# Optimization experiments

Hardware: AMD Instinct MI355X
Metric: run time of the kernel (lower is better)

The kernel has to match this reference:

```python
import jax, jax.numpy as jnp
import numpy as np

BN_EPS = 1e-5
D_SLICE = 3  # forward slices last (neighbor) dim to :3 (d=3 in original code)


def _conv_bn_relu(x, W, b, gamma, beta):
    # x: (B, Cin, N, K) ; W: (Cout, Cin) ; 1x1 Conv2d + eval-mode BatchNorm(mean=0, var=1) + ReLU
    y = jnp.einsum('oi,bink->bonk', W, x) + b[:, None, None]
    y = gamma[:, None, None] * (y / jnp.sqrt(1.0 + BN_EPS)) + beta[:, None, None]
    return jax.nn.relu(y)


def setup_inputs() -> dict:
    key = jax.random.key(0)
    ks = jax.random.split(key, 16)
    B, N, K, C = 4, 32768, 16, 64
    mlp = [128, 64, 64]
    cin = C + 4  # feature + relation (diff_xyz 3 + distance 1)
    inp = {
        'src_xyz': jax.random.normal(ks[0], (B, 3, N, K), dtype=jnp.float32),
        'tgt_xyz': jax.random.normal(ks[1], (B, 3, N), dtype=jnp.float32),
        'feature': jax.random.normal(ks[2], (B, C, N, K), dtype=jnp.float32),
    }
    c_prev = cin
    for i, c_out in enumerate(mlp):
        scale = 1.0 / np.sqrt(c_prev)
        inp[f'W{i+1}'] = jax.random.uniform(ks[3 + 4 * i], (c_out, c_prev), minval=-scale, maxval=scale, dtype=jnp.float32)
        inp[f'b{i+1}'] = jax.random.uniform(ks[4 + 4 * i], (c_out,), minval=-scale, maxval=scale, dtype=jnp.float32)
        inp[f'g{i+1}'] = jnp.ones((c_out,), dtype=jnp.float32)
        inp[f'be{i+1}'] = jnp.zeros((c_out,), dtype=jnp.float32)
        c_prev = c_out
    return inp


def reference(src_xyz, tgt_xyz, feature, W1, b1, g1, be1, W2, b2, g2, be2, W3, b3, g3, be3):
    # relation feature on first D_SLICE neighbors (faithful to feature[:,:,:,:d], d=3)
    diff_xyz = src_xyz[:, :, :, :D_SLICE] - tgt_xyz[:, :, :, None]        # (B,3,N,3)
    distance = jnp.sum(diff_xyz ** 2, axis=1, keepdims=True)             # (B,1,N,3)
    x = jnp.concatenate([feature[:, :, :, :D_SLICE], diff_xyz, distance], axis=1)  # (B,C+4,N,3)
    x = _conv_bn_relu(x, W1, b1, g1, be1)
    x = _conv_bn_relu(x, W2, b2, g2, be2)
    x = _conv_bn_relu(x, W3, b3, g3, be3)
    return jnp.sum(x, axis=3)  # reduction='sum' over neighbor dim -> (B,64,N)
```

## Files before the change

### kernel.cpp

```cpp
#include <hip/hip_runtime.h>
#include <math.h>

typedef __attribute__((ext_vector_type(8))) short short8;
typedef __attribute__((ext_vector_type(4))) short short4v;
typedef __attribute__((ext_vector_type(4))) float f32x4;
typedef __attribute__((ext_vector_type(16))) float f32x16;
typedef _Float16 half8 __attribute__((ext_vector_type(8)));

constexpr int BLOCK = 512;
constexpr int B_ = 4, C_ = 64, N_ = 32768, K_ = 16;
constexpr int P_ = 32;
constexpr int NFRAG = 44;
constexpr int BIAS_OFF = NFRAG * 512;

constexpr int ZOFF = 9 * 768;
constexpr int XSZ  = 6920;
constexpr int H2STR = 776;

__device__ __forceinline__ short f16bits(float v) {
    return (short)__builtin_bit_cast(unsigned short, (_Float16)v);
}

__device__ __forceinline__ f32x16 mm32h(half8 a, half8 b, f32x16 c) {
    return __builtin_amdgcn_mfma_f32_32x32x16_f16(a, b, c, 0, 0, 0);
}
__device__ __forceinline__ f32x4 mm16h(half8 a, half8 b, f32x4 c) {
    return __builtin_amdgcn_mfma_f32_16x16x32_f16(a, b, c, 0, 0, 0);
}

__global__ void prep_wfrags(const float* __restrict__ W1, const float* __restrict__ g1,
                            const float* __restrict__ b1, const float* __restrict__ be1,
                            const float* __restrict__ W2, const float* __restrict__ g2,
                            const float* __restrict__ b2, const float* __restrict__ be2,
                            const float* __restrict__ W3, const float* __restrict__ g3,
                            const float* __restrict__ b3, const float* __restrict__ be3,
                            unsigned short* __restrict__ wf)
{
    const int gid = blockIdx.x * 256 + threadIdx.x;
    const float RS = 1.0f / sqrtf(1.0f + 1e-5f);
    const int NT = NFRAG * 64;
    if (gid < NT) {
        const int f = gid >> 6, l = gid & 63;
        const float *W, *g; int CI, co, kb;
        if (f < 20)      { W = W1; g = g1; CI = 68;
                           co = (f / 5) * 32 + (l & 31);        kb = (f % 5) * 16 + (l >> 5) * 8; }
        else if (f < 36) { W = W2; g = g2; CI = 128;
                           co = ((f - 20) / 8) * 32 + (l & 31); kb = ((f - 20) % 8) * 16 + (l >> 5) * 8; }
        else             { W = W3; g = g3; CI = 64;
                           co = ((f - 36) / 2) * 16 + (l & 15); kb = ((f - 36) % 2) * 32 + (l >> 4) * 8; }
        const float gs = g[co] * RS;
        short8 h8;
#pragma unroll
        for (int j = 0; j < 8; ++j) {
            const int k = kb + j;
            const float w = (k < CI) ? W[(size_t)co * CI + k] * gs : 0.0f;
            h8[j] = f16bits(w);
        }
        *reinterpret_cast<short8*>(wf + (size_t)f * 512 + l * 8) = h8;
    } else if (gid < NT + 256) {
        const int c = gid - NT;
        float* fb = reinterpret_cast<float*>(wf + BIAS_OFF);
        if (c < 128)      fb[c] = b1[c] * (g1[c] * RS) + be1[c];
        else if (c < 192) { const int q = c - 128; fb[c] = b2[q] * (g2[q] * RS) + be2[q]; }
        else              { const int q = c - 192; fb[c] = b3[q] * (g3[q] * RS) + be3[q]; }
    }
}

__device__ __forceinline__ half8 ldfrag(const unsigned short* __restrict__ wf,
                                        int f, int l) {
    return __builtin_bit_cast(half8,
        *reinterpret_cast<const short8*>(wf + (size_t)f * 512 + l * 8));
}

__global__ __launch_bounds__(BLOCK, 8)
void mvp_mfma(const float* __restrict__ src, const float* __restrict__ tgt,
              const float* __restrict__ feat,
              const unsigned short* __restrict__ wf,
              float* __restrict__ out)
{
    __shared__ __align__(16) unsigned short xa[XSZ];
    __shared__ __align__(16) unsigned short h1f[16*768];

    const int tid = threadIdx.x;
    const int w   = tid >> 6;
    const int l   = tid & 63;
    const int b   = blockIdx.x >> 10;
    const int n0  = (blockIdx.x & 1023) << 5;

    unsigned short* h2f = xa;

    float4 pf[4];
#pragma unroll
    for (int it = 0; it < 4; ++it) {
        const int idx = tid + it * BLOCK;
        const int c = idx >> 5, p = idx & 31;
        pf[it] = *reinterpret_cast<const float4*>(
            feat + ((size_t)(b*C_ + c) * N_ + (n0 + p)) * K_);
    }
    float rl[6];
    if (tid < 96) {
        const int p = tid & 31, k = tid >> 5, n = n0 + p;
        rl[0] = src[((size_t)(b*3+0)*N_ + n)*K_ + k];
        rl[1] = src[((size_t)(b*3+1)*N_ + n)*K_ + k];
        rl[2] = src[((size_t)(b*3+2)*N_ + n)*K_ + k];
        rl[3] = tgt[(size_t)(b*3+0)*N_ + n];
        rl[4] = tgt[(size_t)(b*3+1)*N_ + n];
        rl[5] = tgt[(size_t)(b*3+2)*N_ + n];
    }

    if (tid < 96) {
        const int o = (8*96 + tid) * 8 + 4;
        *reinterpret_cast<short4v*>(&xa[o]) = short4v{0,0,0,0};
    } else if (tid == 96) {
        *reinterpret_cast<short8*>(xa + ZOFF) = short8{0,0,0,0,0,0,0,0};
    }

#pragma unroll
    for (int it = 0; it < 4; ++it) {
        const int idx = tid + it * BLOCK;
        const int c = idx >> 5, p = idx & 31;
        const float v[3] = {pf[it].x, pf[it].y, pf[it].z};
#pragma unroll
        for (int k = 0; k < 3; ++k)
            xa[((c >> 3)*96 + k*32 + p)*8 + (c & 7)] = (unsigned short)f16bits(v[k]);
    }
    if (tid < 96) {
        const int p = tid & 31, k = tid >> 5;
        const float d0 = rl[0]-rl[3], d1 = rl[1]-rl[4], d2 = rl[2]-rl[5];
        const float d[4] = {d0, d1, d2, d0*d0 + d1*d1 + d2*d2};
        const int base = (8*96 + k*32 + p)*8;
#pragma unroll
        for (int j = 0; j < 4; ++j)
            xa[base + j] = (unsigned short)f16bits(d[j]);
    }
    __syncthreads();

    const int hi32 = l >> 5, c32 = l & 31;
    const int lq = l >> 4, lr = l & 15, rq = lq << 2;
    const float* fb = reinterpret_cast<const float*>(wf + BIAS_OFF);

    {
        const int npass = (w < 4) ? 2 : 1;
        for (int pass = 0; pass < npass; ++pass) {
            const int t = pass ? (8 + w) : w;
            const int m = t / 3, n = t % 3;
            const int col = n*32 + c32;
            half8 ah[5];
#pragma unroll
            for (int ks = 0; ks < 5; ++ks) ah[ks] = ldfrag(wf, m*5 + ks, l);
            f32x16 acc;
#pragma unroll
            for (int j = 0; j < 16; ++j) acc[j] = 0.0f;
#pragma unroll
            for (int ks = 0; ks < 4; ++ks) {
                const int so = ((ks*2 + hi32)*96 + col)*8;
                const half8 bh = __builtin_bit_cast(half8,
                    *reinterpret_cast<const short8*>(&xa[so]));
                acc = mm32h(ah[ks], bh, acc);
            }
            {
                const int so = hi32 ? ZOFF : (8*96 + col)*8;
                const half8 bh = __builtin_bit_cast(half8,
                    *reinterpret_cast<const short8*>(&xa[so]));
                acc = mm32h(ah[4], bh, acc);
            }
#pragma unroll
            for (int g = 0; g < 4; ++g) {
                const int co0 = m*32 + 8*g + 4*hi32;
                const float4 bb = *reinterpret_cast<const float4*>(fb + co0);
                const float bbv[4] = {bb.x, bb.y, bb.z, bb.w};
                short4v h4;
#pragma unroll
                for (int r = 0; r < 4; ++r)
                    h4[r] = f16bits(fmaxf(acc[g*4 + r] + bbv[r], 0.0f));
                const int so = ((m*4 + g)*96 + col)*8 + 4*hi32;
                *reinterpret_cast<short4v*>(&h1f[so]) = h4;
            }
        }
    }
    __syncthreads();

    if (w < 6) {
        const int m = w / 3, n = w % 3;
        const int col = n*32 + c32;
        f32x16 acc;
#pragma unroll
        for (int j = 0; j < 16; ++j) acc[j] = 0.0f;
#pragma unroll
        for (int ks = 0; ks < 8; ++ks) {
            const half8 ah = ldfrag(wf, 20 + m*8 + ks, l);
            const int so = ((ks*2 + hi32)*96 + col)*8;
            const half8 bh = __builtin_bit_cast(half8,
                *reinterpret_cast<const short8*>(&h1f[so]));
            acc = mm32h(ah, bh, acc);
        }
#pragma unroll
        for (int g = 0; g < 4; ++g) {
            const int co0 = m*32 + 8*g + 4*hi32;
            const float4 bb = *reinterpret_cast<const float4*>(fb + 128 + co0);
            const float bbv[4] = {bb.x, bb.y, bb.z, bb.w};
            short4v h4;
#pragma unroll
            for (int r = 0; r < 4; ++r)
                h4[r] = f16bits(fmaxf(acc[g*4 + r] + bbv[r], 0.0f));
            const int so = (m*4 + g)*H2STR + col*8 + 4*hi32;
            *reinterpret_cast<short4v*>(&h2f[so]) = h4;
        }
    }
    __syncthreads();

    {
        const int m = w >> 1, hh = w & 1;
        half8 ah[2];
#pragma unroll
        for (int ks = 0; ks < 2; ++ks) ah[ks] = ldfrag(wf, 36 + m*2 + ks, l);
        f32x4 acc3[3] = {f32x4{0,0,0,0}, f32x4{0,0,0,0}, f32x4{0,0,0,0}};
#pragma unroll
        for (int ks = 0; ks < 2; ++ks) {
#pragma unroll
            for (int t = 0; t < 3; ++t) {
                const int so = (ks*4 + lq)*H2STR + (t*32 + hh*16 + lr)*8;
                const half8 bh = __builtin_bit_cast(half8,
                    *reinterpret_cast<const short8*>(&h2f[so]));
                acc3[t] = mm16h(ah[ks], bh, acc3[t]);
            }
        }
        const int co0 = m*16 + rq;
        const float4 bb = *reinterpret_cast<const float4*>(fb + 192 + co0);
        const float bbv[4] = {bb.x, bb.y, bb.z, bb.w};
#pragma unroll
        for (int r = 0; r < 4; ++r) {
            float s = 0.0f;
#pragma unroll
            for (int t = 0; t < 3; ++t) s += fmaxf(acc3[t][r] + bbv[r], 0.0f);
            out[(size_t)(b*64 + co0 + r) * N_ + n0 + hh*16 + lr] = s;
        }
    }
}

extern "C" void kernel_launch(void* const* d_in, const int* in_sizes, int n_in,
                              void* d_out, int out_size, void* d_ws, size_t ws_size,
                              hipStream_t stream) {
    const float* src  = (const float*)d_in[0];
    const float* tgt  = (const float*)d_in[1];
    const float* feat = (const float*)d_in[2];
    const float* W1 = (const float*)d_in[3];
    const float* b1 = (const float*)d_in[4];
    const float* g1 = (const float*)d_in[5];
    const float* be1= (const float*)d_in[6];
    const float* W2 = (const float*)d_in[7];
    const float* b2 = (const float*)d_in[8];
    const float* g2 = (const float*)d_in[9];
    const float* be2= (const float*)d_in[10];
    const float* W3 = (const float*)d_in[11];
    const float* b3 = (const float*)d_in[12];
    const float* g3 = (const float*)d_in[13];
    const float* be3= (const float*)d_in[14];
    float* out = (float*)d_out;
    unsigned short* wfrag = (unsigned short*)d_ws;

    prep_wfrags<<<12, 256, 0, stream>>>(W1, g1, b1, be1, W2, g2, b2, be2,
                                        W3, g3, b3, be3, wfrag);

    const int grid = B_ * (N_ / P_);
    mvp_mfma<<<grid, BLOCK, 0, stream>>>(src, tgt, feat, wfrag, out);
}
```

Baseline: 137.6 us.

## Process two 32-point tiles per block with all feature loads issued up front

Each block now handles 64 points as two 32-point tiles, and the grid is halved. The global feature, src and tgt loads for both tiles are issued together at kernel start into a double-buffered LDS input area. The three MLP layers then run on each tile in turn. This raises memory-level parallelism per block and spreads the per-block setup over more work, at the cost of more LDS and registers per block and a lower occupancy target in launch bounds (8 to 6).

```diff
diff --git a/kernel.cpp b/kernel.cpp
--- a/kernel.cpp
+++ b/kernel.cpp
@@ -72,34 +72,36 @@
         *reinterpret_cast<const short8*>(wf + (size_t)f * 512 + l * 8));
 }
 
-__global__ __launch_bounds__(BLOCK, 8)
+__global__ __launch_bounds__(BLOCK, 6)
 void mvp_mfma(const float* __restrict__ src, const float* __restrict__ tgt,
               const float* __restrict__ feat,
               const unsigned short* __restrict__ wf,
               float* __restrict__ out)
 {
-    __shared__ __align__(16) unsigned short xa[XSZ];
+    __shared__ __align__(16) unsigned short xa[2][XSZ];
     __shared__ __align__(16) unsigned short h1f[16*768];
 
     const int tid = threadIdx.x;
     const int w   = tid >> 6;
     const int l   = tid & 63;
-    const int b   = blockIdx.x >> 10;
-    const int n0  = (blockIdx.x & 1023) << 5;
-
-    unsigned short* h2f = xa;
-
-    float4 pf[4];
-#pragma unroll
-    for (int it = 0; it < 4; ++it) {
-        const int idx = tid + it * BLOCK;
-        const int c = idx >> 5, p = idx & 31;
-        pf[it] = *reinterpret_cast<const float4*>(
-            feat + ((size_t)(b*C_ + c) * N_ + (n0 + p)) * K_);
-    }
+    const int b   = blockIdx.x >> 9;
+    const int n0  = (blockIdx.x & 511) << 6;
+
+    float4 pf[8];
+#pragma unroll
+    for (int t = 0; t < 2; ++t)
+#pragma unroll
+        for (int it = 0; it < 4; ++it) {
+            const int idx = tid + it * BLOCK;
+            const int c = idx >> 5, p = idx & 31;
+            pf[t*4 + it] = *reinterpret_cast<const float4*>(
+                feat + ((size_t)(b*C_ + c) * N_ + (n0 + t*32 + p)) * K_);
+        }
     float rl[6];
-    if (tid < 96) {
-        const int p = tid & 31, k = tid >> 5, n = n0 + p;
+    int tt = 0, cc = 0;
+    if (tid < 192) {
+        tt = tid / 96; cc = tid % 96;
+        const int p = cc & 31, k = cc >> 5, n = n0 + tt*32 + p;
         rl[0] = src[((size_t)(b*3+0)*N_ + n)*K_ + k];
         rl[1] = src[((size_t)(b*3+1)*N_ + n)*K_ + k];
         rl[2] = src[((size_t)(b*3+2)*N_ + n)*K_ + k];
@@ -110,28 +112,33 @@
 
     if (tid < 96) {
         const int o = (8*96 + tid) * 8 + 4;
-        *reinterpret_cast<short4v*>(&xa[o]) = short4v{0,0,0,0};
+        *reinterpret_cast<short4v*>(&xa[0][o]) = short4v{0,0,0,0};
+        *reinterpret_cast<short4v*>(&xa[1][o]) = short4v{0,0,0,0};
     } else if (tid == 96) {
-        *reinterpret_cast<short8*>(xa + ZOFF) = short8{0,0,0,0,0,0,0,0};
-    }
-
-#pragma unroll
-    for (int it = 0; it < 4; ++it) {
-        const int idx = tid + it * BLOCK;
-        const int c = idx >> 5, p = idx & 31;
-        const float v[3] = {pf[it].x, pf[it].y, pf[it].z};
-#pragma unroll
-        for (int k = 0; k < 3; ++k)
-            xa[((c >> 3)*96 + k*32 + p)*8 + (c & 7)] = (unsigned short)f16bits(v[k]);
-    }
-    if (tid < 96) {
-        const int p = tid & 31, k = tid >> 5;
+        *reinterpret_cast<short8*>(&xa[0][ZOFF]) = short8{0,0,0,0,0,0,0,0};
+        *reinterpret_cast<short8*>(&xa[1][ZOFF]) = short8{0,0,0,0,0,0,0,0};
+    }
+
+#pragma unroll
+    for (int t = 0; t < 2; ++t)
+#pragma unroll
+        for (int it = 0; it < 4; ++it) {
+            const int idx = tid + it * BLOCK;
+            const int c = idx >> 5, p = idx & 31;
+            const float4 f = pf[t*4 + it];
+            const float v[3] = {f.x, f.y, f.z};
+#pragma unroll
+            for (int k = 0; k < 3; ++k)
+                xa[t][((c >> 3)*96 + k*32 + p)*8 + (c & 7)] = (unsigned short)f16bits(v[k]);
+        }
+    if (tid < 192) {
+        const int p = cc & 31, k = cc >> 5;
         const float d0 = rl[0]-rl[3], d1 = rl[1]-rl[4], d2 = rl[2]-rl[5];
         const float d[4] = {d0, d1, d2, d0*d0 + d1*d1 + d2*d2};
         const int base = (8*96 + k*32 + p)*8;
 #pragma unroll
         for (int j = 0; j < 4; ++j)
-            xa[base + j] = (unsigned short)f16bits(d[j]);
+            xa[tt][base + j] = (unsigned short)f16bits(d[j]);
     }
     __syncthreads();
 
@@ -139,101 +146,107 @@
     const int lq = l >> 4, lr = l & 15, rq = lq << 2;
     const float* fb = reinterpret_cast<const float*>(wf + BIAS_OFF);
 
-    {
-        const int npass = (w < 4) ? 2 : 1;
-        for (int pass = 0; pass < npass; ++pass) {
-            const int t = pass ? (8 + w) : w;
-            const int m = t / 3, n = t % 3;
+#pragma unroll 1
+    for (int t = 0; t < 2; ++t) {
+        const unsigned short* xat = &xa[t][0];
+        unsigned short* h2f = &xa[t][0];
+
+        {
+            const int npass = (w < 4) ? 2 : 1;
+            for (int pass = 0; pass < npass; ++pass) {
+                const int tt1 = pass ? (8 + w) : w;
+                const int m = tt1 / 3, n = tt1 % 3;
+                const int col = n*32 + c32;
+                half8 ah[5];
+#pragma unroll
+                for (int ks = 0; ks < 5; ++ks) ah[ks] = ldfrag(wf, m*5 + ks, l);
+                f32x16 acc;
+#pragma unroll
+                for (int j = 0; j < 16; ++j) acc[j] = 0.0f;
+#pragma unroll
+                for (int ks = 0; ks < 4; ++ks) {
+                    const int so = ((ks*2 + hi32)*96 + col)*8;
+                    const half8 bh = __builtin_bit_cast(half8,
+                        *reinterpret_cast<const short8*>(&xat[so]));
+                    acc = mm32h(ah[ks], bh, acc);
+                }
+                {
+                    const int so = hi32 ? ZOFF : (8*96 + col)*8;
+                    const half8 bh = __builtin_bit_cast(half8,
+                        *reinterpret_cast<const short8*>(&xat[so]));
+                    acc = mm32h(ah[4], bh, acc);
+                }
+#pragma unroll
+                for (int g = 0; g < 4; ++g) {
+                    const int co0 = m*32 + 8*g + 4*hi32;
+                    const float4 bb = *reinterpret_cast<const float4*>(fb + co0);
+                    const float bbv[4] = {bb.x, bb.y, bb.z, bb.w};
+                    short4v h4;
+#pragma unroll
+                    for (int r = 0; r < 4; ++r)
+                        h4[r] = f16bits(fmaxf(acc[g*4 + r] + bbv[r], 0.0f));
+                    const int so = ((m*4 + g)*96 + col)*8 + 4*hi32;
+                    *reinterpret_cast<short4v*>(&h1f[so]) = h4;
+                }
+            }
+        }
+        __syncthreads();
+
+        if (w < 6) {
+            const int m = w / 3, n = w % 3;
             const int col = n*32 + c32;
-            half8 ah[5];
-#pragma unroll
-            for (int ks = 0; ks < 5; ++ks) ah[ks] = ldfrag(wf, m*5 + ks, l);
             f32x16 acc;
 #pragma unroll
             for (int j = 0; j < 16; ++j) acc[j] = 0.0f;
 #pragma unroll
-            for (int ks = 0; ks < 4; ++ks) {
+            for (int ks = 0; ks < 8; ++ks) {
+                const half8 ah = ldfrag(wf, 20 + m*8 + ks, l);
                 const int so = ((ks*2 + hi32)*96 + col)*8;
                 const half8 bh = __builtin_bit_cast(half8,
-                    *reinterpret_cast<const short8*>(&xa[so]));
-                acc = mm32h(ah[ks], bh, acc);
-            }
-            {
-                const int so = hi32 ? ZOFF : (8*96 + col)*8;
-                const half8 bh = __builtin_bit_cast(half8,
-                    *reinterpret_cast<const short8*>(&xa[so]));
-                acc = mm32h(ah[4], bh, acc);
+                    *reinterpret_cast<const short8*>(&h1f[so]));
+                acc = mm32h(ah, bh, acc);
             }
 #pragma unroll
             for (int g = 0; g < 4; ++g) {
                 const int co0 = m*32 + 8*g + 4*hi32;
-                const float4 bb = *reinterpret_cast<const float4*>(fb + co0);
+                const float4 bb = *reinterpret_cast<const float4*>(fb + 128 + co0);
                 const float bbv[4] = {bb.x, bb.y, bb.z, bb.w};
                 short4v h4;
 #pragma unroll
                 for (int r = 0; r < 4; ++r)
                     h4[r] = f16bits(fmaxf(acc[g*4 + r] + bbv[r], 0.0f));
-                const int so = ((m*4 + g)*96 + col)*8 + 4*hi32;
-                *reinterpret_cast<short4v*>(&h1f[so]) = h4;
-            }
-        }
-    }
-    __syncthreads();
-
-    if (w < 6) {
-        const int m = w / 3, n = w % 3;
-        const int col = n*32 + c32;
-        f32x16 acc;
-#pragma unroll
-        for (int j = 0; j < 16; ++j) acc[j] = 0.0f;
-#pragma unroll
-        for (int ks = 0; ks < 8; ++ks) {
-            const half8 ah = ldfrag(wf, 20 + m*8 + ks, l);
-            const int so = ((ks*2 + hi32)*96 + col)*8;
-            const half8 bh = __builtin_bit_cast(half8,
-                *reinterpret_cast<const short8*>(&h1f[so]));
-            acc = mm32h(ah, bh, acc);
-        }
-#pragma unroll
-        for (int g = 0; g < 4; ++g) {
-            const int co0 = m*32 + 8*g + 4*hi32;
-            const float4 bb = *reinterpret_cast<const float4*>(fb + 128 + co0);
+                const int so = (m*4 + g)*H2STR + col*8 + 4*hi32;
+                *reinterpret_cast<short4v*>(&h2f[so]) = h4;
+            }
+        }
+        __syncthreads();
+
+        {
+            const int m = w >> 1, hh = w & 1;
+            half8 ah[2];
+#pragma unroll
+            for (int ks = 0; ks < 2; ++ks) ah[ks] = ldfrag(wf, 36 + m*2 + ks, l);
+            f32x4 acc3[3] = {f32x4{0,0,0,0}, f32x4{0,0,0,0}, f32x4{0,0,0,0}};
+#pragma unroll
+            for (int ks = 0; ks < 2; ++ks) {
+#pragma unroll
+                for (int tk = 0; tk < 3; ++tk) {
+                    const int so = (ks*4 + lq)*H2STR + (tk*32 + hh*16 + lr)*8;
+                    const half8 bh = __builtin_bit_cast(half8,
+                        *reinterpret_cast<const short8*>(&h2f[so]));
+                    acc3[tk] = mm16h(ah[ks], bh, acc3[tk]);
+                }
+            }
+            const int co0 = m*16 + rq;
+            const float4 bb = *reinterpret_cast<const float4*>(fb + 192 + co0);
             const float bbv[4] = {bb.x, bb.y, bb.z, bb.w};
-            short4v h4;
-#pragma unroll
-            for (int r = 0; r < 4; ++r)
-                h4[r] = f16bits(fmaxf(acc[g*4 + r] + bbv[r], 0.0f));
-            const int so = (m*4 + g)*H2STR + col*8 + 4*hi32;
-            *reinterpret_cast<short4v*>(&h2f[so]) = h4;
-        }
-    }
-    __syncthreads();
-
-    {
-        const int m = w >> 1, hh = w & 1;
-        half8 ah[2];
-#pragma unroll
-        for (int ks = 0; ks < 2; ++ks) ah[ks] = ldfrag(wf, 36 + m*2 + ks, l);
-        f32x4 acc3[3] = {f32x4{0,0,0,0}, f32x4{0,0,0,0}, f32x4{0,0,0,0}};
-#pragma unroll
-        for (int ks = 0; ks < 2; ++ks) {
-#pragma unroll
-            for (int t = 0; t < 3; ++t) {
-                const int so = (ks*4 + lq)*H2STR + (t*32 + hh*16 + lr)*8;
-                const half8 bh = __builtin_bit_cast(half8,
-                    *reinterpret_cast<const short8*>(&h2f[so]));
-                acc3[t] = mm16h(ah[ks], bh, acc3[t]);
-            }
-        }
-        const int co0 = m*16 + rq;
-        const float4 bb = *reinterpret_cast<const float4*>(fb + 192 + co0);
-        const float bbv[4] = {bb.x, bb.y, bb.z, bb.w};
-#pragma unroll
-        for (int r = 0; r < 4; ++r) {
-            float s = 0.0f;
-#pragma unroll
-            for (int t = 0; t < 3; ++t) s += fmaxf(acc3[t][r] + bbv[r], 0.0f);
-            out[(size_t)(b*64 + co0 + r) * N_ + n0 + hh*16 + lr] = s;
+#pragma unroll
+            for (int r = 0; r < 4; ++r) {
+                float s = 0.0f;
+#pragma unroll
+                for (int tk = 0; tk < 3; ++tk) s += fmaxf(acc3[tk][r] + bbv[r], 0.0f);
+                out[(size_t)(b*64 + co0 + r) * N_ + n0 + t*32 + hh*16 + lr] = s;
+            }
         }
     }
 }
@@ -262,6 +275,6 @@
     prep_wfrags<<<12, 256, 0, stream>>>(W1, g1, b1, be1, W2, g2, b2, be2,
                                         W3, g3, b3, be3, wfrag);
 
-    const int grid = B_ * (N_ / P_);
+    const int grid = B_ * (N_ / 64);
     mvp_mfma<<<grid, BLOCK, 0, stream>>>(src, tgt, feat, wfrag, out);
 }
```

Result: slower. 242.2 us (+76.0%).

## Split fused kernel into input-packing kernel and MLP kernel via workspace

Applied to the files above, without the earlier changes.

Splits the single fused kernel into two. The first gathers features and relation terms, converts them to fp16 and writes them to global workspace already in the MFMA fragment layout. The second reads that packed layout straight from global memory as the B operand of the first layer and runs the three MFMA layers. The aim is to separate the latency-bound gather from the compute, at the cost of an extra global round-trip of about 15 KB per block plus a second launch. The fused path is kept as a fallback when the workspace is too small.

```diff
diff --git a/kernel.cpp b/kernel.cpp
--- a/kernel.cpp
+++ b/kernel.cpp
@@ -17,10 +17,13 @@
 constexpr int XSZ  = 6920;
 constexpr int H2STR = 776;
 
+constexpr int XG_SHORTS = 10 * 96 * 8;
+constexpr size_t XG_OFF = 65536;
+constexpr int NBLK = B_ * (N_ / P_);
+
 __device__ __forceinline__ short f16bits(float v) {
     return (short)__builtin_bit_cast(unsigned short, (_Float16)v);
 }
-
 __device__ __forceinline__ f32x16 mm32h(half8 a, half8 b, f32x16 c) {
     return __builtin_amdgcn_mfma_f32_32x32x16_f16(a, b, c, 0, 0, 0);
 }
@@ -73,6 +76,176 @@
 }
 
 __global__ __launch_bounds__(BLOCK, 8)
+void prep_x(const float* __restrict__ src, const float* __restrict__ tgt,
+            const float* __restrict__ feat, unsigned short* __restrict__ xg)
+{
+    __shared__ __align__(16) unsigned short xa[XG_SHORTS];
+
+    const int tid = threadIdx.x;
+    const int b   = blockIdx.x >> 10;
+    const int n0  = (blockIdx.x & 1023) << 5;
+
+    float4 pf[4];
+#pragma unroll
+    for (int it = 0; it < 4; ++it) {
+        const int idx = tid + it * BLOCK;
+        const int c = idx >> 5, p = idx & 31;
+        pf[it] = *reinterpret_cast<const float4*>(
+            feat + ((size_t)(b*C_ + c) * N_ + (n0 + p)) * K_);
+    }
+    float rl[6];
+    if (tid < 96) {
+        const int p = tid & 31, k = tid >> 5, n = n0 + p;
+        rl[0] = src[((size_t)(b*3+0)*N_ + n)*K_ + k];
+        rl[1] = src[((size_t)(b*3+1)*N_ + n)*K_ + k];
+        rl[2] = src[((size_t)(b*3+2)*N_ + n)*K_ + k];
+        rl[3] = tgt[(size_t)(b*3+0)*N_ + n];
+        rl[4] = tgt[(size_t)(b*3+1)*N_ + n];
+        rl[5] = tgt[(size_t)(b*3+2)*N_ + n];
+    }
+    if (tid < 96) {
+        *reinterpret_cast<short4v*>(&xa[(8*96 + tid)*8 + 4]) = short4v{0,0,0,0};
+        *reinterpret_cast<short8*>(&xa[(9*96 + tid)*8])      = short8{0,0,0,0,0,0,0,0};
+    }
+#pragma unroll
+    for (int it = 0; it < 4; ++it) {
+        const int idx = tid + it * BLOCK;
+        const int c = idx >> 5, p = idx & 31;
+        const float v[3] = {pf[it].x, pf[it].y, pf[it].z};
+#pragma unroll
+        for (int k = 0; k < 3; ++k)
+            xa[((c >> 3)*96 + k*32 + p)*8 + (c & 7)] = (unsigned short)f16bits(v[k]);
+    }
+    if (tid < 96) {
+        const int p = tid & 31, k = tid >> 5;
+        const float d0 = rl[0]-rl[3], d1 = rl[1]-rl[4], d2 = rl[2]-rl[5];
+        const float d[4] = {d0, d1, d2, d0*d0 + d1*d1 + d2*d2};
+        const int base = (8*96 + k*32 + p)*8;
+#pragma unroll
+        for (int j = 0; j < 4; ++j)
+            xa[base + j] = (unsigned short)f16bits(d[j]);
+    }
+    __syncthreads();
+
+    short8* dst = reinterpret_cast<short8*>(xg + (size_t)blockIdx.x * XG_SHORTS);
+    const short8* srcv = reinterpret_cast<const short8*>(xa);
+    for (int i = tid; i < XG_SHORTS/8; i += BLOCK) dst[i] = srcv[i];
+}
+
+__global__ __launch_bounds__(BLOCK, 8)
+void mvp_mlp(const unsigned short* __restrict__ xg,
+             const unsigned short* __restrict__ wf,
+             float* __restrict__ out)
+{
+    __shared__ __align__(16) unsigned short h1f[16*768];
+    __shared__ __align__(16) unsigned short h2f[6208];
+
+    const int tid = threadIdx.x;
+    const int w   = tid >> 6;
+    const int l   = tid & 63;
+    const int b   = blockIdx.x >> 10;
+    const int n0  = (blockIdx.x & 1023) << 5;
+
+    const unsigned short* xb = xg + (size_t)blockIdx.x * XG_SHORTS;
+
+    const int hi32 = l >> 5, c32 = l & 31;
+    const int lq = l >> 4, lr = l & 15, rq = lq << 2;
+    const float* fb = reinterpret_cast<const float*>(wf + BIAS_OFF);
+
+    {
+        const int npass = (w < 4) ? 2 : 1;
+        for (int pass = 0; pass < npass; ++pass) {
+            const int t = pass ? (8 + w) : w;
+            const int m = t / 3, n = t % 3;
+            const int col = n*32 + c32;
+            half8 ah[5];
+#pragma unroll
+            for (int ks = 0; ks < 5; ++ks) ah[ks] = ldfrag(wf, m*5 + ks, l);
+            f32x16 acc;
+#pragma unroll
+            for (int j = 0; j < 16; ++j) acc[j] = 0.0f;
+#pragma unroll
+            for (int ks = 0; ks < 5; ++ks) {
+                const int so = ((ks*2 + hi32)*96 + col)*8;
+                const half8 bh = __builtin_bit_cast(half8,
+                    *reinterpret_cast<const short8*>(&xb[so]));
+                acc = mm32h(ah[ks], bh, acc);
+            }
+#pragma unroll
+            for (int g = 0; g < 4; ++g) {
+                const int co0 = m*32 + 8*g + 4*hi32;
+                const float4 bb = *reinterpret_cast<const float4*>(fb + co0);
+                const float bbv[4] = {bb.x, bb.y, bb.z, bb.w};
+                short4v h4;
+#pragma unroll
+                for (int r = 0; r < 4; ++r)
+                    h4[r] = f16bits(fmaxf(acc[g*4 + r] + bbv[r], 0.0f));
+                const int so = ((m*4 + g)*96 + col)*8 + 4*hi32;
+                *reinterpret_cast<short4v*>(&h1f[so]) = h4;
+            }
+        }
+    }
+    __syncthreads();
+
+    if (w < 6) {
+        const int m = w / 3, n = w % 3;
+        const int col = n*32 + c32;
+        f32x16 acc;
+#pragma unroll
+        for (int j = 0; j < 16; ++j) acc[j] = 0.0f;
+#pragma unroll
+        for (int ks = 0; ks < 8; ++ks) {
+            const half8 ah = ldfrag(wf, 20 + m*8 + ks, l);
+            const int so = ((ks*2 + hi32)*96 + col)*8;
+            const half8 bh = __builtin_bit_cast(half8,
+                *reinterpret_cast<const short8*>(&h1f[so]));
+            acc = mm32h(ah, bh, acc);
+        }
+#pragma unroll
+        for (int g = 0; g < 4; ++g) {
+            const int co0 = m*32 + 8*g + 4*hi32;
+            const float4 bb = *reinterpret_cast<const float4*>(fb + 128 + co0);
+            const float bbv[4] = {bb.x, bb.y, bb.z, bb.w};
+            short4v h4;
+#pragma unroll
+            for (int r = 0; r < 4; ++r)
+                h4[r] = f16bits(fmaxf(acc[g*4 + r] + bbv[r], 0.0f));
+            const int so = (m*4 + g)*H2STR + col*8 + 4*hi32;
+            *reinterpret_cast<short4v*>(&h2f[so]) = h4;
+        }
+    }
+    __syncthreads();
+
+    {
+        const int m = w >> 1, hh = w & 1;
+        half8 ah[2];
+#pragma unroll
+        for (int ks = 0; ks < 2; ++ks) ah[ks] = ldfrag(wf, 36 + m*2 + ks, l);
+        f32x4 acc3[3] = {f32x4{0,0,0,0}, f32x4{0,0,0,0}, f32x4{0,0,0,0}};
+#pragma unroll
+        for (int ks = 0; ks < 2; ++ks) {
+#pragma unroll
+            for (int t = 0; t < 3; ++t) {
+                const int so = (ks*4 + lq)*H2STR + (t*32 + hh*16 + lr)*8;
+                const half8 bh = __builtin_bit_cast(half8,
+                    *reinterpret_cast<const short8*>(&h2f[so]));
+                acc3[t] = mm16h(ah[ks], bh, acc3[t]);
+            }
+        }
+        const int co0 = m*16 + rq;
+        const float4 bb = *reinterpret_cast<const float4*>(fb + 192 + co0);
+        const float bbv[4] = {bb.x, bb.y, bb.z, bb.w};
+#pragma unroll
+        for (int r = 0; r < 4; ++r) {
+            float s = 0.0f;
+#pragma unroll
+            for (int t = 0; t < 3; ++t) s += fmaxf(acc3[t][r] + bbv[r], 0.0f);
+            out[(size_t)(b*64 + co0 + r) * N_ + n0 + hh*16 + lr] = s;
+        }
+    }
+}
+
+__global__ __launch_bounds__(BLOCK, 8)
 void mvp_mfma(const float* __restrict__ src, const float* __restrict__ tgt,
               const float* __restrict__ feat,
               const unsigned short* __restrict__ wf,
@@ -107,14 +280,12 @@
         rl[4] = tgt[(size_t)(b*3+1)*N_ + n];
         rl[5] = tgt[(size_t)(b*3+2)*N_ + n];
     }
-
     if (tid < 96) {
         const int o = (8*96 + tid) * 8 + 4;
         *reinterpret_cast<short4v*>(&xa[o]) = short4v{0,0,0,0};
     } else if (tid == 96) {
         *reinterpret_cast<short8*>(xa + ZOFF) = short8{0,0,0,0,0,0,0,0};
     }
-
 #pragma unroll
     for (int it = 0; it < 4; ++it) {
         const int idx = tid + it * BLOCK;
@@ -262,6 +433,12 @@
     prep_wfrags<<<12, 256, 0, stream>>>(W1, g1, b1, be1, W2, g2, b2, be2,
                                         W3, g3, b3, be3, wfrag);
 
-    const int grid = B_ * (N_ / P_);
-    mvp_mfma<<<grid, BLOCK, 0, stream>>>(src, tgt, feat, wfrag, out);
-}
+    const size_t need = XG_OFF + (size_t)NBLK * XG_SHORTS * 2;
+    if (ws_size >= need) {
+        unsigned short* xg = (unsigned short*)((char*)d_ws + XG_OFF);
+        prep_x<<<NBLK, BLOCK, 0, stream>>>(src, tgt, feat, xg);
+        mvp_mlp<<<NBLK, BLOCK, 0, stream>>>(xg, wfrag, out);
+    } else {
+        mvp_mfma<<<NBLK, BLOCK, 0, stream>>>(src, tgt, feat, wfrag, out);
+    }
+}
```

Result: slower. 170.6 us (+24.0%).

## Chain MLP layers in registers via lane shuffles, drop intermediate LDS stages

Applied to the files above, without the earlier changes.

Each block now handles 64 points, and each wave owns 32 columns (8 points × 4 padded neighbor slots) for all three layers. Layer outputs are repacked from MFMA accumulator layout into B-operand layout with cross-half-wave shuffles, so the h1/h2 shared-memory buffers and two barriers go away. Layer 3 switches to 32x32 MFMA, and the neighbor sum is done with lane shuffles. This trades some wasted compute on a padded fourth neighbor slot, plus more register pressure (launch bounds lowered to 6), for less LDS traffic and fewer syncs.

```diff
diff --git a/kernel.cpp b/kernel.cpp
--- a/kernel.cpp
+++ b/kernel.cpp
@@ -3,29 +3,27 @@
 
 typedef __attribute__((ext_vector_type(8))) short short8;
 typedef __attribute__((ext_vector_type(4))) short short4v;
-typedef __attribute__((ext_vector_type(4))) float f32x4;
+typedef __attribute__((ext_vector_type(4))) unsigned u32x4;
 typedef __attribute__((ext_vector_type(16))) float f32x16;
 typedef _Float16 half8 __attribute__((ext_vector_type(8)));
 
 constexpr int BLOCK = 512;
 constexpr int B_ = 4, C_ = 64, N_ = 32768, K_ = 16;
-constexpr int P_ = 32;
 constexpr int NFRAG = 44;
 constexpr int BIAS_OFF = NFRAG * 512;
 
-constexpr int ZOFF = 9 * 768;
-constexpr int XSZ  = 6920;
-constexpr int H2STR = 776;
+constexpr int XCOLS = 256;
+constexpr int XSZ   = 10 * XCOLS * 8;
 
 __device__ __forceinline__ short f16bits(float v) {
     return (short)__builtin_bit_cast(unsigned short, (_Float16)v);
 }
-
 __device__ __forceinline__ f32x16 mm32h(half8 a, half8 b, f32x16 c) {
     return __builtin_amdgcn_mfma_f32_32x32x16_f16(a, b, c, 0, 0, 0);
 }
-__device__ __forceinline__ f32x4 mm16h(half8 a, half8 b, f32x4 c) {
-    return __builtin_amdgcn_mfma_f32_16x16x32_f16(a, b, c, 0, 0, 0);
+__device__ __forceinline__ half8 mkh8(const unsigned a[4]) {
+    u32x4 t = {a[0], a[1], a[2], a[3]};
+    return __builtin_bit_cast(half8, t);
 }
 
 __global__ void prep_wfrags(const float* __restrict__ W1, const float* __restrict__ g1,
@@ -47,7 +45,7 @@
         else if (f < 36) { W = W2; g = g2; CI = 128;
                            co = ((f - 20) / 8) * 32 + (l & 31); kb = ((f - 20) % 8) * 16 + (l >> 5) * 8; }
         else             { W = W3; g = g3; CI = 64;
-                           co = ((f - 36) / 2) * 16 + (l & 15); kb = ((f - 36) % 2) * 32 + (l >> 4) * 8; }
+                           co = ((f - 36) >> 2) * 32 + (l & 31); kb = ((f - 36) & 3) * 16 + (l >> 5) * 8; }
         const float gs = g[co] * RS;
         short8 h8;
 #pragma unroll
@@ -72,168 +70,164 @@
         *reinterpret_cast<const short8*>(wf + (size_t)f * 512 + l * 8));
 }
 
-__global__ __launch_bounds__(BLOCK, 8)
-void mvp_mfma(const float* __restrict__ src, const float* __restrict__ tgt,
-              const float* __restrict__ feat,
-              const unsigned short* __restrict__ wf,
-              float* __restrict__ out)
+__device__ __forceinline__ void d2b(const f32x16& acc, const float* __restrict__ fb,
+                                    int co0, int hi32, int l,
+                                    unsigned out0[4], unsigned out1[4])
+{
+    unsigned a[8];
+#pragma unroll
+    for (int g = 0; g < 4; ++g) {
+        const float4 bb = *reinterpret_cast<const float4*>(fb + co0 + 8*g + 4*hi32);
+        const float v0 = fmaxf(acc[g*4+0] + bb.x, 0.f);
+        const float v1 = fmaxf(acc[g*4+1] + bb.y, 0.f);
+        const float v2 = fmaxf(acc[g*4+2] + bb.z, 0.f);
+        const float v3 = fmaxf(acc[g*4+3] + bb.w, 0.f);
+        a[g*2+0] = (unsigned)(unsigned short)f16bits(v0) |
+                   ((unsigned)(unsigned short)f16bits(v1) << 16);
+        a[g*2+1] = (unsigned)(unsigned short)f16bits(v2) |
+                   ((unsigned)(unsigned short)f16bits(v3) << 16);
+    }
+    unsigned s[8];
+#pragma unroll
+    for (int i = 0; i < 8; ++i) s[i] = (unsigned)__shfl((int)a[i], l ^ 32, 64);
+    if (hi32 == 0) {
+        out0[0]=a[0]; out0[1]=a[1]; out0[2]=s[0]; out0[3]=s[1];
+        out1[0]=a[4]; out1[1]=a[5]; out1[2]=s[4]; out1[3]=s[5];
+    } else {
+        out0[0]=s[2]; out0[1]=s[3]; out0[2]=a[2]; out0[3]=a[3];
+        out1[0]=s[6]; out1[1]=s[7]; out1[2]=a[6]; out1[3]=a[7];
+    }
+}
+
+__global__ __launch_bounds__(BLOCK, 6)
+void mvp_fused(const float* __restrict__ src, const float* __restrict__ tgt,
+               const float* __restrict__ feat,
+               const unsigned short* __restrict__ wf,
+               float* __restrict__ out)
 {
     __shared__ __align__(16) unsigned short xa[XSZ];
-    __shared__ __align__(16) unsigned short h1f[16*768];
 
     const int tid = threadIdx.x;
     const int w   = tid >> 6;
     const int l   = tid & 63;
-    const int b   = blockIdx.x >> 10;
-    const int n0  = (blockIdx.x & 1023) << 5;
-
-    unsigned short* h2f = xa;
-
-    float4 pf[4];
-#pragma unroll
-    for (int it = 0; it < 4; ++it) {
-        const int idx = tid + it * BLOCK;
-        const int c = idx >> 5, p = idx & 31;
-        pf[it] = *reinterpret_cast<const float4*>(
-            feat + ((size_t)(b*C_ + c) * N_ + (n0 + p)) * K_);
-    }
-    float rl[6];
-    if (tid < 96) {
-        const int p = tid & 31, k = tid >> 5, n = n0 + p;
-        rl[0] = src[((size_t)(b*3+0)*N_ + n)*K_ + k];
-        rl[1] = src[((size_t)(b*3+1)*N_ + n)*K_ + k];
-        rl[2] = src[((size_t)(b*3+2)*N_ + n)*K_ + k];
-        rl[3] = tgt[(size_t)(b*3+0)*N_ + n];
-        rl[4] = tgt[(size_t)(b*3+1)*N_ + n];
-        rl[5] = tgt[(size_t)(b*3+2)*N_ + n];
-    }
-
-    if (tid < 96) {
-        const int o = (8*96 + tid) * 8 + 4;
-        *reinterpret_cast<short4v*>(&xa[o]) = short4v{0,0,0,0};
-    } else if (tid == 96) {
-        *reinterpret_cast<short8*>(xa + ZOFF) = short8{0,0,0,0,0,0,0,0};
-    }
-
-#pragma unroll
-    for (int it = 0; it < 4; ++it) {
-        const int idx = tid + it * BLOCK;
-        const int c = idx >> 5, p = idx & 31;
-        const float v[3] = {pf[it].x, pf[it].y, pf[it].z};
-#pragma unroll
-        for (int k = 0; k < 3; ++k)
-            xa[((c >> 3)*96 + k*32 + p)*8 + (c & 7)] = (unsigned short)f16bits(v[k]);
-    }
-    if (tid < 96) {
-        const int p = tid & 31, k = tid >> 5;
-        const float d0 = rl[0]-rl[3], d1 = rl[1]-rl[4], d2 = rl[2]-rl[5];
-        const float d[4] = {d0, d1, d2, d0*d0 + d1*d1 + d2*d2};
-        const int base = (8*96 + k*32 + p)*8;
+    const int b   = blockIdx.x >> 9;
+    const int n0  = (blockIdx.x & 511) << 6;
+
+    {
+        if (tid < 256)
+            *reinterpret_cast<short8*>(&xa[(9*XCOLS + tid)*8]) = short8{0,0,0,0,0,0,0,0};
+        else {
+            const int gc = tid - 256;
+            *reinterpret_cast<short4v*>(&xa[(8*XCOLS + gc)*8 + 4]) = short4v{0,0,0,0};
+        }
+        const int fr = tid >> 6, q = tid & 63;
+        const int gpad = (q >> 3)*32 + (q & 7)*4 + 3;
+        *reinterpret_cast<short8*>(&xa[(fr*XCOLS + gpad)*8]) = short8{0,0,0,0,0,0,0,0};
+        if (tid < 64) {
+            const int gp = (tid >> 3)*32 + (tid & 7)*4 + 3;
+            *reinterpret_cast<short4v*>(&xa[(8*XCOLS + gp)*8]) = short4v{0,0,0,0};
+        }
+    }
+#pragma unroll
+    for (int grp = 0; grp < 2; ++grp) {
+        float4 pf[4];
+#pragma unroll
+        for (int it = 0; it < 4; ++it) {
+            const int idx = tid + (grp*4 + it) * BLOCK;
+            const int c = idx >> 6, pt = idx & 63;
+            pf[it] = *reinterpret_cast<const float4*>(
+                feat + ((size_t)(b*C_ + c) * N_ + (n0 + pt)) * K_);
+        }
+#pragma unroll
+        for (int it = 0; it < 4; ++it) {
+            const int idx = tid + (grp*4 + it) * BLOCK;
+            const int c = idx >> 6, pt = idx & 63;
+            const float v[3] = {pf[it].x, pf[it].y, pf[it].z};
+#pragma unroll
+            for (int k = 0; k < 3; ++k) {
+                const int gcol = (pt >> 3)*32 + (pt & 7)*4 + k;
+                xa[((c >> 3)*XCOLS + gcol)*8 + (c & 7)] = (unsigned short)f16bits(v[k]);
+            }
+        }
+    }
+    if (tid < 192) {
+        const int pt = tid / 3, k = tid % 3;
+        const int n = n0 + pt;
+        const float d0 = src[((size_t)(b*3+0)*N_ + n)*K_ + k] - tgt[(size_t)(b*3+0)*N_ + n];
+        const float d1 = src[((size_t)(b*3+1)*N_ + n)*K_ + k] - tgt[(size_t)(b*3+1)*N_ + n];
+        const float d2 = src[((size_t)(b*3+2)*N_ + n)*K_ + k] - tgt[(size_t)(b*3+2)*N_ + n];
+        const float dd[4] = {d0, d1, d2, d0*d0 + d1*d1 + d2*d2};
+        const int gcol = (pt >> 3)*32 + (pt & 7)*4 + k;
+        const int base = (8*XCOLS + gcol)*8;
 #pragma unroll
         for (int j = 0; j < 4; ++j)
-            xa[base + j] = (unsigned short)f16bits(d[j]);
+            xa[base + j] = (unsigned short)f16bits(dd[j]);
     }
     __syncthreads();
 
-    const int hi32 = l >> 5, c32 = l & 31;
-    const int lq = l >> 4, lr = l & 15, rq = lq << 2;
+    const int hi32 = l >> 5;
+    const int c32  = l & 31;
     const float* fb = reinterpret_cast<const float*>(wf + BIAS_OFF);
-
-    {
-        const int npass = (w < 4) ? 2 : 1;
-        for (int pass = 0; pass < npass; ++pass) {
-            const int t = pass ? (8 + w) : w;
-            const int m = t / 3, n = t % 3;
-            const int col = n*32 + c32;
-            half8 ah[5];
-#pragma unroll
-            for (int ks = 0; ks < 5; ++ks) ah[ks] = ldfrag(wf, m*5 + ks, l);
-            f32x16 acc;
-#pragma unroll
-            for (int j = 0; j < 16; ++j) acc[j] = 0.0f;
-#pragma unroll
-            for (int ks = 0; ks < 4; ++ks) {
-                const int so = ((ks*2 + hi32)*96 + col)*8;
-                const half8 bh = __builtin_bit_cast(half8,
-                    *reinterpret_cast<const short8*>(&xa[so]));
-                acc = mm32h(ah[ks], bh, acc);
-            }
-            {
-                const int so = hi32 ? ZOFF : (8*96 + col)*8;
-                const half8 bh = __builtin_bit_cast(half8,
-                    *reinterpret_cast<const short8*>(&xa[so]));
-                acc = mm32h(ah[4], bh, acc);
-            }
-#pragma unroll
-            for (int g = 0; g < 4; ++g) {
-                const int co0 = m*32 + 8*g + 4*hi32;
-                const float4 bb = *reinterpret_cast<const float4*>(fb + co0);
-                const float bbv[4] = {bb.x, bb.y, bb.z, bb.w};
-                short4v h4;
-#pragma unroll
-                for (int r = 0; r < 4; ++r)
-                    h4[r] = f16bits(fmaxf(acc[g*4 + r] + bbv[r], 0.0f));
-                const int so = ((m*4 + g)*96 + col)*8 + 4*hi32;
-                *reinterpret_cast<short4v*>(&h1f[so]) = h4;
-            }
-        }
-    }
-    __syncthreads();
-
-    if (w < 6) {
-        const int m = w / 3, n = w % 3;
-        const int col = n*32 + c32;
+    const int xcol = w*32 + c32;
+
+    unsigned h1B[8][4];
+#pragma unroll
+    for (int m = 0; m < 4; ++m) {
+        f32x16 acc;
+#pragma unroll
+        for (int j = 0; j < 16; ++j) acc[j] = 0.0f;
+#pragma unroll
+        for (int ks = 0; ks < 5; ++ks) {
+            const half8 ah = ldfrag(wf, m*5 + ks, l);
+            const half8 bh = __builtin_bit_cast(half8,
+                *reinterpret_cast<const short8*>(&xa[((ks*2 + hi32)*XCOLS + xcol)*8]));
+            acc = mm32h(ah, bh, acc);
+        }
+        d2b(acc, fb, m*32, hi32, l, h1B[2*m], h1B[2*m+1]);
+    }
+
+    unsigned h2B[4][4];
+#pragma unroll
+    for (int m = 0; m < 2; ++m) {
         f32x16 acc;
 #pragma unroll
         for (int j = 0; j < 16; ++j) acc[j] = 0.0f;
 #pragma unroll
         for (int ks = 0; ks < 8; ++ks) {
             const half8 ah = ldfrag(wf, 20 + m*8 + ks, l);
-            const int so = ((ks*2 + hi32)*96 + col)*8;
-            const half8 bh = __builtin_bit_cast(half8,
-                *reinterpret_cast<const short8*>(&h1f[so]));
-            acc = mm32h(ah, bh, acc);
+            acc = mm32h(ah, mkh8(h1B[ks]), acc);
+        }
+        d2b(acc, fb + 128, m*32, hi32, l, h2B[2*m], h2B[2*m+1]);
+    }
+
+    const int lbase = l & ~3;
+    const int lp    = c32 >> 2;
+#pragma unroll
+    for (int m = 0; m < 2; ++m) {
+        f32x16 acc;
+#pragma unroll
+        for (int j = 0; j < 16; ++j) acc[j] = 0.0f;
+#pragma unroll
+        for (int ks = 0; ks < 4; ++ks) {
+            const half8 ah = ldfrag(wf, 36 + m*4 + ks, l);
+            acc = mm32h(ah, mkh8(h2B[ks]), acc);
         }
 #pragma unroll
         for (int g = 0; g < 4; ++g) {
-            const int co0 = m*32 + 8*g + 4*hi32;
-            const float4 bb = *reinterpret_cast<const float4*>(fb + 128 + co0);
+            const float4 bb = *reinterpret_cast<const float4*>(
+                fb + 192 + m*32 + 8*g + 4*hi32);
             const float bbv[4] = {bb.x, bb.y, bb.z, bb.w};
-            short4v h4;
-#pragma unroll
-            for (int r = 0; r < 4; ++r)
-                h4[r] = f16bits(fmaxf(acc[g*4 + r] + bbv[r], 0.0f));
-            const int so = (m*4 + g)*H2STR + col*8 + 4*hi32;
-            *reinterpret_cast<short4v*>(&h2f[so]) = h4;
-        }
-    }
-    __syncthreads();
-
-    {
-        const int m = w >> 1, hh = w & 1;
-        half8 ah[2];
-#pragma unroll
-        for (int ks = 0; ks < 2; ++ks) ah[ks] = ldfrag(wf, 36 + m*2 + ks, l);
-        f32x4 acc3[3] = {f32x4{0,0,0,0}, f32x4{0,0,0,0}, f32x4{0,0,0,0}};
-#pragma unroll
-        for (int ks = 0; ks < 2; ++ks) {
-#pragma unroll
-            for (int t = 0; t < 3; ++t) {
-                const int so = (ks*4 + lq)*H2STR + (t*32 + hh*16 + lr)*8;
-                const half8 bh = __builtin_bit_cast(half8,
-                    *reinterpret_cast<const short8*>(&h2f[so]));
-                acc3[t] = mm16h(ah[ks], bh, acc3[t]);
+#pragma unroll
+            for (int r = 0; r < 4; ++r) {
+                const float v = fmaxf(acc[g*4 + r] + bbv[r], 0.0f);
+                const float t = __shfl(v, lbase, 64)
+                              + __shfl(v, lbase + 1, 64)
+                              + __shfl(v, lbase + 2, 64);
+                if ((l & 3) == 0) {
+                    const int row = m*32 + 8*g + 4*hi32 + r;
+                    out[(size_t)(b*64 + row) * N_ + n0 + w*8 + lp] = t;
+                }
             }
-        }
-        const int co0 = m*16 + rq;
-        const float4 bb = *reinterpret_cast<const float4*>(fb + 192 + co0);
-        const float bbv[4] = {bb.x, bb.y, bb.z, bb.w};
-#pragma unroll
-        for (int r = 0; r < 4; ++r) {
-            float s = 0.0f;
-#pragma unroll
-            for (int t = 0; t < 3; ++t) s += fmaxf(acc3[t][r] + bbv[r], 0.0f);
-            out[(size_t)(b*64 + co0 + r) * N_ + n0 + hh*16 + lr] = s;
         }
     }
 }
@@ -262,6 +256,6 @@
     prep_wfrags<<<12, 256, 0, stream>>>(W1, g1, b1, be1, W2, g2, b2, be2,
                                         W3, g3, b3, be3, wfrag);
 
-    const int grid = B_ * (N_ / P_);
-    mvp_mfma<<<grid, BLOCK, 0, stream>>>(src, tgt, feat, wfrag, out);
-}
+    const int grid = B_ * (N_ / 64);
+    mvp_fused<<<grid, BLOCK, 0, stream>>>(src, tgt, feat, wfrag, out);
+}
```

After: 170.8 us. 1.24x slower.
